# Optimization experiments

Measured on AMD Instinct MI355X. Metric: run time of the kernel, lower is better.

## Reference

```python
import jax, jax.numpy as jnp
import numpy as np

B, K, L, P = 8192, 25, 25, 1
BN_EPS = 1e-5


def setup_inputs() -> dict:
    key = jax.random.key(0)
    ks = jax.random.split(key, 12)
    s = 0.3  # weight init scale
    return {
        "x": jax.random.normal(ks[0], (B, L), dtype=jnp.float32),
        "gamma": jnp.ones((L,), dtype=jnp.float32),
        "bn_bias": jnp.zeros((L,), dtype=jnp.float32),
        "W1": s * jax.random.normal(ks[1], (K, L, P, 8), dtype=jnp.float32),
        "b1": s * jax.random.normal(ks[2], (K, L, P, 8), dtype=jnp.float32),
        "W2": s * jax.random.normal(ks[3], (K, L, P, 8, 8), dtype=jnp.float32),
        "b2": s * jax.random.normal(ks[4], (K, L, P, 8), dtype=jnp.float32),
        "W3": s * jax.random.normal(ks[5], (K, L, P, 6, 8), dtype=jnp.float32),
        "b3": s * jax.random.normal(ks[6], (K, L, P, 6), dtype=jnp.float32),
        "W4": s * jax.random.normal(ks[7], (K, L, P, 6), dtype=jnp.float32),
        "b4": s * jax.random.normal(ks[8], (K, L, P), dtype=jnp.float32),
        "alpha": jax.random.uniform(ks[9], (L, K), dtype=jnp.float32),
        "beta": jax.random.normal(ks[10], (K,), dtype=jnp.float32),
    }


def reference(x, gamma, bn_bias, W1, b1, W2, b2, W3, b3, W4, b4, alpha, beta):
    # BatchNorm1d(L) in training mode: biased batch statistics over the batch dim
    mean = jnp.mean(x, axis=0)
    var = jnp.var(x, axis=0)
    xn = (x - mean) * jax.lax.rsqrt(var + BN_EPS) * gamma + bn_bias  # [B, L]

    # Batched tiny MLPs: one 1->8->8->6->1 net per (k, l, p)
    h1 = jax.nn.relu(jnp.einsum('bl,klph->bklph', xn, W1) + b1)          # [B,K,L,P,8]
    h2 = jax.nn.relu(jnp.einsum('bklph,klpih->bklpi', h1, W2) + b2)      # [B,K,L,P,8]
    h3 = jax.nn.relu(jnp.einsum('bklpi,klpji->bklpj', h2, W3) + b3)      # [B,K,L,P,6]
    f = jnp.einsum('bklpj,klpj->bklp', h3, W4) + b4                      # [B,K,L,P]
    out = jnp.swapaxes(jnp.sum(f, axis=-1), 1, 2)                        # [B,L,K] (sum over p)
    return beta + jnp.sum(out * alpha[None, :, :], axis=1)               # [B,K]
```

## Files before the change

kernel.cpp:

```cpp
#include <hip/hip_runtime.h>

#define BATCH  8192
#define KK     25
#define LL     25
#define BN_EPS 1e-5f
#define PREPB  32
#define LG     5
#define NLG    (LL / LG)
#define VB     4
#define WSP    80

#define WS_PART   0
#define WS_SCALE  1600
#define WS_SHIFT  1632
#define WS_XT     2048
#define WS_FP     (WS_XT + LL * BATCH)
#define WS_END    (WS_FP + NLG * KK * BATCH)

typedef _Float16 h2v __attribute__((ext_vector_type(2)));

static __device__ __forceinline__ h2v pk_fma_wl(h2v a, h2v w, h2v c) {
    h2v d;
    asm("v_pk_fma_f16 %0, %1, %2, %3 op_sel:[0,0,0] op_sel_hi:[1,0,1]"
        : "=v"(d) : "v"(a), "v"(w), "v"(c));
    return d;
}
static __device__ __forceinline__ h2v pk_fma_wh(h2v a, h2v w, h2v c) {
    h2v d;
    asm("v_pk_fma_f16 %0, %1, %2, %3 op_sel:[0,1,0] op_sel_hi:[1,1,1]"
        : "=v"(d) : "v"(a), "v"(w), "v"(c));
    return d;
}
static __device__ __forceinline__ h2v pk_fma_wl_cl(h2v a, h2v w, h2v c) {
    h2v d;
    asm("v_pk_fma_f16 %0, %1, %2, %3 op_sel:[0,0,0] op_sel_hi:[1,0,0]"
        : "=v"(d) : "v"(a), "v"(w), "v"(c));
    return d;
}
static __device__ __forceinline__ h2v pk_fma_wl_ch(h2v a, h2v w, h2v c) {
    h2v d;
    asm("v_pk_fma_f16 %0, %1, %2, %3 op_sel:[0,0,1] op_sel_hi:[1,0,1]"
        : "=v"(d) : "v"(a), "v"(w), "v"(c));
    return d;
}
static __device__ __forceinline__ h2v pk_fma_wh_ch(h2v a, h2v w, h2v c) {
    h2v d;
    asm("v_pk_fma_f16 %0, %1, %2, %3 op_sel:[0,1,1] op_sel_hi:[1,1,1]"
        : "=v"(d) : "v"(a), "v"(w), "v"(c));
    return d;
}
static __device__ __forceinline__ h2v pk_max(h2v a, h2v b) {
    h2v d;
    asm("v_pk_max_f16 %0, %1, %2" : "=v"(d) : "v"(a), "v"(b));
    return d;
}
static __device__ __forceinline__ h2v pack2(float a, float b) {
    h2v r; r.x = (_Float16)a; r.y = (_Float16)b; return r;
}

__global__ __launch_bounds__(256) void prep_kernel(
    const float* __restrict__ x,
    float* __restrict__ xT,
    float* __restrict__ part)
{
    __shared__ float xs[256 * LL];
    const int tid = threadIdx.x;
    const int b0  = blockIdx.x * 256;

    const float* src = x + (size_t)b0 * LL;
    #pragma unroll
    for (int i = 0; i < LL; ++i)
        xs[i * 256 + tid] = src[i * 256 + tid];
    __syncthreads();

    #pragma unroll
    for (int l = 0; l < LL; ++l)
        xT[l * BATCH + b0 + tid] = xs[tid * LL + l];

    float s = 0.f, s2 = 0.f;
    if (tid < 200) {
        const int l = tid % LL;
        const int g = tid / LL;
        #pragma unroll
        for (int r = 0; r < 32; ++r) {
            const float v = xs[(g * 32 + r) * LL + l];
            s += v;
            s2 = fmaf(v, v, s2);
        }
    }
    __syncthreads();
    if (tid < 200) { xs[tid] = s; xs[200 + tid] = s2; }
    __syncthreads();

    if (tid < 50) {
        const int c = tid;
        float t = 0.f;
        if (c < LL) {
            #pragma unroll
            for (int g = 0; g < 8; ++g) t += xs[g * LL + c];
        } else {
            #pragma unroll
            for (int g = 0; g < 8; ++g) t += xs[200 + g * LL + (c - LL)];
        }
        part[blockIdx.x * 50 + c] = t;
    }
}

__global__ __launch_bounds__(256) void eval_kernel(
    const float* __restrict__ xT,
    const float* __restrict__ W1, const float* __restrict__ b1,
    const float* __restrict__ W2, const float* __restrict__ b2,
    const float* __restrict__ W3, const float* __restrict__ b3,
    const float* __restrict__ W4, const float* __restrict__ b4,
    const float* __restrict__ alpha,
    const float* __restrict__ part,
    const float* __restrict__ gamma,
    const float* __restrict__ bn_bias,
    float* __restrict__ fp)
{
    __shared__ h2v   wl[LG * WSP];
    __shared__ float sss[2 * LG];
    __shared__ float tmp[2 * LG];

    const int tid = threadIdx.x;
    const int k   = blockIdx.y;
    const int g   = blockIdx.z;
    const int l0  = g * LG;
    const int kl0 = k * LL + l0;
    const int b   = (blockIdx.x * 256 + tid) * VB;

    if (tid < 160) {
        const int j = tid >> 5, p = tid & 31;
        const float* s = W2 + (kl0 + j) * 64 + 2 * p;
        wl[j * WSP + 8 + p] = pack2(s[0], s[1]);
    }
    if (tid < 120) {
        const int j = tid / 24, p = tid % 24;
        const float* s = W3 + (kl0 + j) * 48 + 2 * p;
        wl[j * WSP + 44 + p] = pack2(s[0], s[1]);
    }
    if (tid < 20) {
        const int j = tid >> 2, p = tid & 3;
        const float* s1 = W1 + (kl0 + j) * 8 + 2 * p;
        const float* t1 = b1 + (kl0 + j) * 8 + 2 * p;
        const float* t2 = b2 + (kl0 + j) * 8 + 2 * p;
        wl[j * WSP +      p] = pack2(s1[0], s1[1]);
        wl[j * WSP +  4 + p] = pack2(t1[0], t1[1]);
        wl[j * WSP + 40 + p] = pack2(t2[0], t2[1]);
    }
    if (tid < 15) {
        const int j = tid / 3, p = tid % 3;
        const float* t3 = b3 + (kl0 + j) * 6 + 2 * p;
        const float* s4 = W4 + (kl0 + j) * 6 + 2 * p;
        wl[j * WSP + 68 + p] = pack2(t3[0], t3[1]);
        wl[j * WSP + 71 + p] = pack2(s4[0], s4[1]);
    }

    if (tid >= 128 && tid < 128 + 2 * LG) {
        const int t2  = tid - 128;
        const int col = (t2 < LG) ? (l0 + t2) : (LL + l0 + t2 - LG);
        float s = 0.f;
        #pragma unroll
        for (int i = 0; i < PREPB; ++i)
            s += part[i * 50 + col];
        tmp[t2] = s;
    }
    __syncthreads();
    if (tid < LG) {
        const float s = tmp[tid], s2 = tmp[LG + tid];
        const float inv_b = 1.f / (float)BATCH;
        const float mean  = s * inv_b;
        const float var   = fmaf(s2, inv_b, -mean * mean);
        const float scale = rsqrtf(var + BN_EPS) * gamma[l0 + tid];
        sss[tid]      = scale;
        sss[LG + tid] = fmaf(-mean, scale, bn_bias[l0 + tid]);
    }
    __syncthreads();

    h2v zero2; zero2.x = (_Float16)0.f; zero2.y = (_Float16)0.f;
    float acc[VB] = {0.f, 0.f, 0.f, 0.f};

    #pragma unroll
    for (int j = 0; j < LG; ++j) {
        const int l = l0 + j;
        const h2v* w = wl + j * WSP;

        const float scale = sss[j];
        const float shift = sss[LG + j];
        const float a     = alpha[l * KK + k];
        const float b4f   = b4[kl0 + j];

        const float4 xv = *(const float4*)&xT[l * BATCH + b];
        h2v xn0, xn1;
        xn0.x = (_Float16)fmaf(xv.x, scale, shift);
        xn0.y = (_Float16)fmaf(xv.y, scale, shift);
        xn1.x = (_Float16)fmaf(xv.z, scale, shift);
        xn1.y = (_Float16)fmaf(xv.w, scale, shift);

        h2v h1a[8], h1b[8];
        #pragma unroll
        for (int p = 0; p < 4; ++p) {
            const h2v wp = w[p], bp = w[4 + p];
            h1a[2*p]   = pk_max(pk_fma_wl_cl(xn0, wp, bp), zero2);
            h1a[2*p+1] = pk_max(pk_fma_wh_ch(xn0, wp, bp), zero2);
            h1b[2*p]   = pk_max(pk_fma_wl_cl(xn1, wp, bp), zero2);
            h1b[2*p+1] = pk_max(pk_fma_wh_ch(xn1, wp, bp), zero2);
        }

        h2v h2a[8], h2b[8];
        #pragma unroll
        for (int i = 0; i < 8; ++i) {
            const h2v bp = w[40 + (i >> 1)];
            const h2v w0 = w[8 + i * 4];
            h2v t0, t1;
            if (i & 1) { t0 = pk_fma_wl_ch(h1a[0], w0, bp);
                         t1 = pk_fma_wl_ch(h1b[0], w0, bp); }
            else       { t0 = pk_fma_wl_cl(h1a[0], w0, bp);
                         t1 = pk_fma_wl_cl(h1b[0], w0, bp); }
            t0 = pk_fma_wh(h1a[1], w0, t0);
            t1 = pk_fma_wh(h1b[1], w0, t1);
            #pragma unroll
            for (int hp = 1; hp < 4; ++hp) {
                const h2v wp = w[8 + i * 4 + hp];
                t0 = pk_fma_wl(h1a[2*hp],   wp, t0);
                t1 = pk_fma_wl(h1b[2*hp],   wp, t1);
                t0 = pk_fma_wh(h1a[2*hp+1], wp, t0);
                t1 = pk_fma_wh(h1b[2*hp+1], wp, t1);
            }
            h2a[i] = pk_max(t0, zero2);
            h2b[i] = pk_max(t1, zero2);
        }

        h2v h3a[6], h3b[6];
        #pragma unroll
        for (int jj = 0; jj < 6; ++jj) {
            const h2v bp = w[68 + (jj >> 1)];
            const h2v w0 = w[44 + jj * 4];
            h2v t0, t1;
            if (jj & 1) { t0 = pk_fma_wl_ch(h2a[0], w0, bp);
                          t1 = pk_fma_wl_ch(h2b[0], w0, bp); }
            else        { t0 = pk_fma_wl_cl(h2a[0], w0, bp);
                          t1 = pk_fma_wl_cl(h2b[0], w0, bp); }
            t0 = pk_fma_wh(h2a[1], w0, t0);
            t1 = pk_fma_wh(h2b[1], w0, t1);
            #pragma unroll
            for (int ip = 1; ip < 4; ++ip) {
                const h2v wp = w[44 + jj * 4 + ip];
                t0 = pk_fma_wl(h2a[2*ip],   wp, t0);
                t1 = pk_fma_wl(h2b[2*ip],   wp, t1);
                t0 = pk_fma_wh(h2a[2*ip+1], wp, t0);
                t1 = pk_fma_wh(h2b[2*ip+1], wp, t1);
            }
            h3a[jj] = pk_max(t0, zero2);
            h3b[jj] = pk_max(t1, zero2);
        }

        h2v fd0 = zero2, fd1 = zero2;
        #pragma unroll
        for (int jp = 0; jp < 3; ++jp) {
            const h2v wp = w[71 + jp];
            fd0 = pk_fma_wl(h3a[2*jp],   wp, fd0);
            fd1 = pk_fma_wl(h3b[2*jp],   wp, fd1);
            fd0 = pk_fma_wh(h3a[2*jp+1], wp, fd0);
            fd1 = pk_fma_wh(h3b[2*jp+1], wp, fd1);
        }
        acc[0] = fmaf(a, b4f + (float)fd0.x, acc[0]);
        acc[1] = fmaf(a, b4f + (float)fd0.y, acc[1]);
        acc[2] = fmaf(a, b4f + (float)fd1.x, acc[2]);
        acc[3] = fmaf(a, b4f + (float)fd1.y, acc[3]);
    }

    float4 o = {acc[0], acc[1], acc[2], acc[3]};
    *(float4*)&fp[(g * KK + k) * BATCH + b] = o;
}

__global__ __launch_bounds__(256) void reduce_kernel(
    const float* __restrict__ fp,
    const float* __restrict__ beta,
    float* __restrict__ out)
{
    const int tid = threadIdx.x;
    const int k   = blockIdx.y;
    const int b   = blockIdx.x * 256 + tid;

    float acc = beta[k];
    #pragma unroll
    for (int g = 0; g < NLG; ++g)
        acc += fp[(g * KK + k) * BATCH + b];
    out[(size_t)b * KK + k] = acc;
}

__device__ __forceinline__ float mlp_eval(
    float xn, int kl,
    const float* __restrict__ W1, const float* __restrict__ b1,
    const float* __restrict__ W2, const float* __restrict__ b2,
    const float* __restrict__ W3, const float* __restrict__ b3,
    const float* __restrict__ W4, const float* __restrict__ b4)
{
    const float* w1  = W1 + kl * 8;
    const float* bb1 = b1 + kl * 8;
    float h1[8];
    #pragma unroll
    for (int h = 0; h < 8; ++h)
        h1[h] = fmaxf(fmaf(xn, w1[h], bb1[h]), 0.f);

    const float* w2  = W2 + kl * 64;
    const float* bb2 = b2 + kl * 8;
    float h2v_[8];
    #pragma unroll
    for (int i = 0; i < 8; ++i) {
        float t = bb2[i];
        #pragma unroll
        for (int h = 0; h < 8; ++h)
            t = fmaf(h1[h], w2[i * 8 + h], t);
        h2v_[i] = fmaxf(t, 0.f);
    }

    const float* w3  = W3 + kl * 48;
    const float* bb3 = b3 + kl * 6;
    float h3[6];
    #pragma unroll
    for (int j = 0; j < 6; ++j) {
        float t = bb3[j];
        #pragma unroll
        for (int i = 0; i < 8; ++i)
            t = fmaf(h2v_[i], w3[j * 8 + i], t);
        h3[j] = fmaxf(t, 0.f);
    }

    const float* w4 = W4 + kl * 6;
    float f = b4[kl];
    #pragma unroll
    for (int j = 0; j < 6; ++j)
        f = fmaf(h3[j], w4[j], f);
    return f;
}

__global__ __launch_bounds__(256) void stats_small_kernel(
    const float* __restrict__ x,
    const float* __restrict__ gamma,
    const float* __restrict__ bn_bias,
    float* __restrict__ ws)
{
    const int l   = blockIdx.x;
    const int tid = threadIdx.x;

    float s = 0.f, s2 = 0.f;
    for (int b = tid; b < BATCH; b += 256) {
        float v = x[b * LL + l];
        s  += v;
        s2  = fmaf(v, v, s2);
    }
    for (int off = 32; off > 0; off >>= 1) {
        s  += __shfl_down(s,  off);
        s2 += __shfl_down(s2, off);
    }
    __shared__ float red[8];
    const int wave = tid >> 6;
    if ((tid & 63) == 0) { red[wave] = s; red[4 + wave] = s2; }
    __syncthreads();
    if (tid == 0) {
        s  = red[0] + red[1] + red[2] + red[3];
        s2 = red[4] + red[5] + red[6] + red[7];
        const float inv_b = 1.f / (float)BATCH;
        float mean = s * inv_b;
        float var  = fmaf(s2, inv_b, -mean * mean);
        float scale = rsqrtf(var + BN_EPS) * gamma[l];
        ws[WS_SCALE + l] = scale;
        ws[WS_SHIFT + l] = fmaf(-mean, scale, bn_bias[l]);
    }
}

__global__ __launch_bounds__(256) void mlp_lds_direct_kernel(
    const float* __restrict__ x,
    const float* __restrict__ W1, const float* __restrict__ b1,
    const float* __restrict__ W2, const float* __restrict__ b2,
    const float* __restrict__ W3, const float* __restrict__ b3,
    const float* __restrict__ W4, const float* __restrict__ b4,
    const float* __restrict__ alpha, const float* __restrict__ beta,
    const float* __restrict__ ws,
    float* __restrict__ out)
{
    __shared__ float xs[256 * LL];
    const int tid = threadIdx.x;
    const int k   = blockIdx.y;
    const int b0  = blockIdx.x * 256;

    const float* xsrc = x + (size_t)b0 * LL;
    #pragma unroll
    for (int i = 0; i < LL; ++i)
        xs[i * 256 + tid] = xsrc[i * 256 + tid];
    __syncthreads();

    float acc = beta[k];
    for (int l = 0; l < LL; ++l) {
        const int kl = k * LL + l;
        const float xn = fmaf(xs[tid * LL + l], ws[WS_SCALE + l], ws[WS_SHIFT + l]);
        const float f  = mlp_eval(xn, kl, W1, b1, W2, b2, W3, b3, W4, b4);
        acc = fmaf(alpha[l * KK + k], f, acc);
    }
    out[(size_t)(b0 + tid) * KK + k] = acc;
}

extern "C" void kernel_launch(void* const* d_in, const int* in_sizes, int n_in,
                              void* d_out, int out_size, void* d_ws, size_t ws_size,
                              hipStream_t stream) {
    const float* x       = (const float*)d_in[0];
    const float* gamma   = (const float*)d_in[1];
    const float* bn_bias = (const float*)d_in[2];
    const float* W1      = (const float*)d_in[3];
    const float* b1      = (const float*)d_in[4];
    const float* W2      = (const float*)d_in[5];
    const float* b2      = (const float*)d_in[6];
    const float* W3      = (const float*)d_in[7];
    const float* b3      = (const float*)d_in[8];
    const float* W4      = (const float*)d_in[9];
    const float* b4      = (const float*)d_in[10];
    const float* alpha   = (const float*)d_in[11];
    const float* beta    = (const float*)d_in[12];

    float* out = (float*)d_out;
    float* ws  = (float*)d_ws;
    float* xT  = ws + WS_XT;
    float* fp  = ws + WS_FP;

    const bool fast = ws_size >= (size_t)WS_END * sizeof(float);

    if (fast) {
        prep_kernel<<<dim3(PREPB), dim3(256), 0, stream>>>(x, xT, ws + WS_PART);
        eval_kernel<<<dim3(BATCH / (256 * VB), KK, NLG), dim3(256), 0, stream>>>(
            xT, W1, b1, W2, b2, W3, b3, W4, b4, alpha,
            ws + WS_PART, gamma, bn_bias, fp);
        reduce_kernel<<<dim3(BATCH / 256, KK), dim3(256), 0, stream>>>(fp, beta, out);
    } else {
        stats_small_kernel<<<dim3(LL), dim3(256), 0, stream>>>(x, gamma, bn_bias, ws);
        mlp_lds_direct_kernel<<<dim3(BATCH / 256, KK), dim3(256), 0, stream>>>(
            x, W1, b1, W2, b2, W3, b3, W4, b4, alpha, beta, ws, out);
    }
}
```

Before: 101.7 us.

## Fuse cross-group reduction into eval kernel via last-block atomic counter

Removes the separate reduce kernel launch. Each eval block writes its partial result, then bumps a per-(batch-tile, k) atomic counter, and the last of the NLG group blocks sums the other partials and writes the final output. The counters are zeroed in the prep kernel. This saves a launch and one read pass over the partials, at the cost of threadfences, an atomic per block, and strided output stores from the last block.

```diff
diff --git a/kernel.cpp b/kernel.cpp
--- a/kernel.cpp
+++ b/kernel.cpp
@@ -8,11 +8,14 @@
 #define LG     5
 #define NLG    (LL / LG)
 #define VB     4
+#define EVT    256
+#define NBX    (BATCH / (EVT * VB))
 #define WSP    80
 
 #define WS_PART   0
 #define WS_SCALE  1600
 #define WS_SHIFT  1632
+#define WS_CNT    1700
 #define WS_XT     2048
 #define WS_FP     (WS_XT + LL * BATCH)
 #define WS_END    (WS_FP + NLG * KK * BATCH)
@@ -66,6 +69,9 @@
     __shared__ float xs[256 * LL];
     const int tid = threadIdx.x;
     const int b0  = blockIdx.x * 256;
+
+    if (blockIdx.x == 0 && tid < NBX * KK)
+        ((int*)part)[WS_CNT + tid] = 0;
 
     const float* src = x + (size_t)b0 * LL;
     #pragma unroll
@@ -116,18 +122,22 @@
     const float* __restrict__ part,
     const float* __restrict__ gamma,
     const float* __restrict__ bn_bias,
-    float* __restrict__ fp)
+    const float* __restrict__ beta,
+    float* __restrict__ fp,
+    int*   __restrict__ cnt,
+    float* __restrict__ out)
 {
     __shared__ h2v   wl[LG * WSP];
     __shared__ float sss[2 * LG];
     __shared__ float tmp[2 * LG];
+    __shared__ int   lastflag;
 
     const int tid = threadIdx.x;
     const int k   = blockIdx.y;
     const int g   = blockIdx.z;
     const int l0  = g * LG;
     const int kl0 = k * LL + l0;
-    const int b   = (blockIdx.x * 256 + tid) * VB;
+    const int b   = (blockIdx.x * EVT + tid) * VB;
 
     if (tid < 160) {
         const int j = tid >> 5, p = tid & 31;
@@ -271,23 +281,29 @@
     }
 
     float4 o = {acc[0], acc[1], acc[2], acc[3]};
-    *(float4*)&fp[(g * KK + k) * BATCH + b] = o;
-}
-
-__global__ __launch_bounds__(256) void reduce_kernel(
-    const float* __restrict__ fp,
-    const float* __restrict__ beta,
-    float* __restrict__ out)
-{
-    const int tid = threadIdx.x;
-    const int k   = blockIdx.y;
-    const int b   = blockIdx.x * 256 + tid;
-
-    float acc = beta[k];
-    #pragma unroll
-    for (int g = 0; g < NLG; ++g)
-        acc += fp[(g * KK + k) * BATCH + b];
-    out[(size_t)b * KK + k] = acc;
+    *(float4*)&fp[((size_t)g * KK + k) * BATCH + b] = o;
+
+    __threadfence();
+    if (tid == 0)
+        lastflag = (atomicAdd(&cnt[blockIdx.x * KK + k], 1) == NLG - 1);
+    __syncthreads();
+
+    if (lastflag) {
+        __threadfence();
+        float s0 = acc[0], s1 = acc[1], s2 = acc[2], s3 = acc[3];
+        #pragma unroll
+        for (int gg = 0; gg < NLG; ++gg) {
+            if (gg == g) continue;
+            const volatile float* src = fp + ((size_t)gg * KK + k) * BATCH + b;
+            s0 += src[0]; s1 += src[1]; s2 += src[2]; s3 += src[3];
+        }
+        const float bk = beta[k];
+        float* dst = out + (size_t)b * KK + k;
+        dst[0]      = bk + s0;
+        dst[KK]     = bk + s1;
+        dst[2 * KK] = bk + s2;
+        dst[3 * KK] = bk + s3;
+    }
 }
 
 __device__ __forceinline__ float mlp_eval(
@@ -423,15 +439,15 @@
     float* ws  = (float*)d_ws;
     float* xT  = ws + WS_XT;
     float* fp  = ws + WS_FP;
+    int*   cnt = (int*)ws + WS_CNT;
 
     const bool fast = ws_size >= (size_t)WS_END * sizeof(float);
 
     if (fast) {
         prep_kernel<<<dim3(PREPB), dim3(256), 0, stream>>>(x, xT, ws + WS_PART);
-        eval_kernel<<<dim3(BATCH / (256 * VB), KK, NLG), dim3(256), 0, stream>>>(
+        eval_kernel<<<dim3(NBX, KK, NLG), dim3(EVT), 0, stream>>>(
             xT, W1, b1, W2, b2, W3, b3, W4, b4, alpha,
-            ws + WS_PART, gamma, bn_bias, fp);
-        reduce_kernel<<<dim3(BATCH / 256, KK), dim3(256), 0, stream>>>(fp, beta, out);
+            ws + WS_PART, gamma, bn_bias, beta, fp, cnt, out);
     } else {
         stats_small_kernel<<<dim3(LL), dim3(256), 0, stream>>>(x, gamma, bn_bias, ws);
         mlp_lds_direct_kernel<<<dim3(BATCH / 256, KK), dim3(256), 0, stream>>>(
```

Result: slower. 183.2 us (+80.1%).

## Fuse L-group partial evaluation and reduction into a single monolithic eval kernel

Applied to the files above, without the earlier changes.

Each block now evaluates all 25 L-slices for its (batch chunk, k) pair, staging all weights for that k in LDS. It then writes the final output directly with beta added, which removes the partial-sum workspace and the separate reduce kernel. This drops a kernel launch and the write and read of the partial buffer. In exchange the grid shrinks fivefold to 200 blocks, fewer than the number of CUs, so occupancy and parallelism fall. The output stores are also strided rather than coalesced.

```diff
diff --git a/kernel.cpp b/kernel.cpp
--- a/kernel.cpp
+++ b/kernel.cpp
@@ -5,17 +5,16 @@
 #define LL     25
 #define BN_EPS 1e-5f
 #define PREPB  32
-#define LG     5
-#define NLG    (LL / LG)
 #define VB     4
+#define EVT    256
+#define NBX    (BATCH / (EVT * VB))
 #define WSP    80
 
 #define WS_PART   0
 #define WS_SCALE  1600
 #define WS_SHIFT  1632
 #define WS_XT     2048
-#define WS_FP     (WS_XT + LL * BATCH)
-#define WS_END    (WS_FP + NLG * KK * BATCH)
+#define WS_END    (WS_XT + LL * BATCH)
 
 typedef _Float16 h2v __attribute__((ext_vector_type(2)));
 
@@ -106,7 +105,7 @@
     }
 }
 
-__global__ __launch_bounds__(256) void eval_kernel(
+__global__ __launch_bounds__(256) void eval_mono_kernel(
     const float* __restrict__ xT,
     const float* __restrict__ W1, const float* __restrict__ b1,
     const float* __restrict__ W2, const float* __restrict__ b2,
@@ -116,79 +115,89 @@
     const float* __restrict__ part,
     const float* __restrict__ gamma,
     const float* __restrict__ bn_bias,
-    float* __restrict__ fp)
+    const float* __restrict__ beta,
+    float* __restrict__ out)
 {
-    __shared__ h2v   wl[LG * WSP];
-    __shared__ float sss[2 * LG];
-    __shared__ float tmp[2 * LG];
-
-    const int tid = threadIdx.x;
-    const int k   = blockIdx.y;
-    const int g   = blockIdx.z;
-    const int l0  = g * LG;
-    const int kl0 = k * LL + l0;
-    const int b   = (blockIdx.x * 256 + tid) * VB;
-
-    if (tid < 160) {
-        const int j = tid >> 5, p = tid & 31;
-        const float* s = W2 + (kl0 + j) * 64 + 2 * p;
-        wl[j * WSP + 8 + p] = pack2(s[0], s[1]);
-    }
-    if (tid < 120) {
-        const int j = tid / 24, p = tid % 24;
-        const float* s = W3 + (kl0 + j) * 48 + 2 * p;
-        wl[j * WSP + 44 + p] = pack2(s[0], s[1]);
-    }
-    if (tid < 20) {
-        const int j = tid >> 2, p = tid & 3;
-        const float* s1 = W1 + (kl0 + j) * 8 + 2 * p;
-        const float* t1 = b1 + (kl0 + j) * 8 + 2 * p;
-        const float* t2 = b2 + (kl0 + j) * 8 + 2 * p;
-        wl[j * WSP +      p] = pack2(s1[0], s1[1]);
-        wl[j * WSP +  4 + p] = pack2(t1[0], t1[1]);
-        wl[j * WSP + 40 + p] = pack2(t2[0], t2[1]);
-    }
-    if (tid < 15) {
-        const int j = tid / 3, p = tid % 3;
-        const float* t3 = b3 + (kl0 + j) * 6 + 2 * p;
-        const float* s4 = W4 + (kl0 + j) * 6 + 2 * p;
-        wl[j * WSP + 68 + p] = pack2(t3[0], t3[1]);
-        wl[j * WSP + 71 + p] = pack2(s4[0], s4[1]);
-    }
-
-    if (tid >= 128 && tid < 128 + 2 * LG) {
-        const int t2  = tid - 128;
-        const int col = (t2 < LG) ? (l0 + t2) : (LL + l0 + t2 - LG);
+    __shared__ h2v   wl[LL * WSP];
+    __shared__ float sss[2 * LL];
+    __shared__ float sab[2 * LL];
+    __shared__ float tmp[2 * LL];
+
+    const int tid   = threadIdx.x;
+    const int k     = blockIdx.y;
+    const int kbase = k * LL;
+    const int b     = (blockIdx.x * EVT + tid) * VB;
+
+    if (tid < 2 * LL) {
         float s = 0.f;
         #pragma unroll
         for (int i = 0; i < PREPB; ++i)
-            s += part[i * 50 + col];
-        tmp[t2] = s;
-    }
-    __syncthreads();
-    if (tid < LG) {
-        const float s = tmp[tid], s2 = tmp[LG + tid];
+            s += part[i * 50 + tid];
+        tmp[tid] = s;
+    }
+    if (tid >= 100 && tid < 100 + LL) {
+        const int l = tid - 100;
+        sab[l]      = alpha[l * KK + k];
+        sab[LL + l] = b4[kbase + l];
+    }
+
+    {
+        const float* src = W2 + (size_t)kbase * 64;
+        for (int idx = tid; idx < 800; idx += EVT) {
+            const int l = idx >> 5, p = idx & 31;
+            const float2 v = *(const float2*)&src[2 * idx];
+            wl[l * WSP + 8 + p] = pack2(v.x, v.y);
+        }
+    }
+    {
+        const float* src = W3 + (size_t)kbase * 48;
+        for (int idx = tid; idx < 600; idx += EVT) {
+            const int l = idx / 24, p = idx - l * 24;
+            const float2 v = *(const float2*)&src[2 * idx];
+            wl[l * WSP + 44 + p] = pack2(v.x, v.y);
+        }
+    }
+    if (tid < 100) {
+        const int l = tid >> 2, p = tid & 3;
+        const float2 v1 = *(const float2*)&W1[kbase * 8 + 2 * tid];
+        const float2 u1 = *(const float2*)&b1[kbase * 8 + 2 * tid];
+        const float2 u2 = *(const float2*)&b2[kbase * 8 + 2 * tid];
+        wl[l * WSP +      p] = pack2(v1.x, v1.y);
+        wl[l * WSP +  4 + p] = pack2(u1.x, u1.y);
+        wl[l * WSP + 40 + p] = pack2(u2.x, u2.y);
+    }
+    if (tid >= 128 && tid < 128 + 75) {
+        const int idx = tid - 128;
+        const int l = idx / 3, p = idx - 3 * l;
+        const float2 u3 = *(const float2*)&b3[kbase * 6 + 2 * idx];
+        const float2 v4 = *(const float2*)&W4[kbase * 6 + 2 * idx];
+        wl[l * WSP + 68 + p] = pack2(u3.x, u3.y);
+        wl[l * WSP + 71 + p] = pack2(v4.x, v4.y);
+    }
+    __syncthreads();
+
+    if (tid < LL) {
+        const float s = tmp[tid], s2 = tmp[LL + tid];
         const float inv_b = 1.f / (float)BATCH;
         const float mean  = s * inv_b;
         const float var   = fmaf(s2, inv_b, -mean * mean);
-        const float scale = rsqrtf(var + BN_EPS) * gamma[l0 + tid];
+        const float scale = rsqrtf(var + BN_EPS) * gamma[tid];
         sss[tid]      = scale;
-        sss[LG + tid] = fmaf(-mean, scale, bn_bias[l0 + tid]);
+        sss[LL + tid] = fmaf(-mean, scale, bn_bias[tid]);
     }
     __syncthreads();
 
     h2v zero2; zero2.x = (_Float16)0.f; zero2.y = (_Float16)0.f;
     float acc[VB] = {0.f, 0.f, 0.f, 0.f};
 
-    #pragma unroll
-    for (int j = 0; j < LG; ++j) {
-        const int l = l0 + j;
-        const h2v* w = wl + j * WSP;
-
-        const float scale = sss[j];
-        const float shift = sss[LG + j];
-        const float a     = alpha[l * KK + k];
-        const float b4f   = b4[kl0 + j];
+    #pragma unroll 5
+    for (int l = 0; l < LL; ++l) {
+        const h2v* w = wl + l * WSP;
+
+        const float scale = sss[l];
+        const float shift = sss[LL + l];
+        const float a     = sab[l];
+        const float b4f   = sab[LL + l];
 
         const float4 xv = *(const float4*)&xT[l * BATCH + b];
         h2v xn0, xn1;
@@ -270,24 +279,12 @@
         acc[3] = fmaf(a, b4f + (float)fd1.y, acc[3]);
     }
 
-    float4 o = {acc[0], acc[1], acc[2], acc[3]};
-    *(float4*)&fp[(g * KK + k) * BATCH + b] = o;
-}
-
-__global__ __launch_bounds__(256) void reduce_kernel(
-    const float* __restrict__ fp,
-    const float* __restrict__ beta,
-    float* __restrict__ out)
-{
-    const int tid = threadIdx.x;
-    const int k   = blockIdx.y;
-    const int b   = blockIdx.x * 256 + tid;
-
-    float acc = beta[k];
-    #pragma unroll
-    for (int g = 0; g < NLG; ++g)
-        acc += fp[(g * KK + k) * BATCH + b];
-    out[(size_t)b * KK + k] = acc;
+    const float bk = beta[k];
+    float* dst = out + (size_t)b * KK + k;
+    dst[0]      = bk + acc[0];
+    dst[KK]     = bk + acc[1];
+    dst[2 * KK] = bk + acc[2];
+    dst[3 * KK] = bk + acc[3];
 }
 
 __device__ __forceinline__ float mlp_eval(
@@ -422,16 +419,14 @@
     float* out = (float*)d_out;
     float* ws  = (float*)d_ws;
     float* xT  = ws + WS_XT;
-    float* fp  = ws + WS_FP;
 
     const bool fast = ws_size >= (size_t)WS_END * sizeof(float);
 
     if (fast) {
         prep_kernel<<<dim3(PREPB), dim3(256), 0, stream>>>(x, xT, ws + WS_PART);
-        eval_kernel<<<dim3(BATCH / (256 * VB), KK, NLG), dim3(256), 0, stream>>>(
+        eval_mono_kernel<<<dim3(NBX, KK), dim3(EVT), 0, stream>>>(
             xT, W1, b1, W2, b2, W3, b3, W4, b4, alpha,
-            ws + WS_PART, gamma, bn_bias, fp);
-        reduce_kernel<<<dim3(BATCH / 256, KK), dim3(256), 0, stream>>>(fp, beta, out);
+            ws + WS_PART, gamma, bn_bias, beta, out);
     } else {
         stats_small_kernel<<<dim3(LL), dim3(256), 0, stream>>>(x, gamma, bn_bias, ws);
         mlp_lds_direct_kernel<<<dim3(BATCH / 256, KK), dim3(256), 0, stream>>>(
```

Result: slower. 130.6 us (+28.4%).
